# Kernel tuning notes

Measured on AMD Instinct MI355X. Metric: run time of the kernel, lower is better.

## Reference

```python
import jax, jax.numpy as jnp
import numpy as np

N_NODES = 50000
N_EDGES = 800000
D_IN = 256
D_HID = 256
N_LAYERS = 3
N_GRAPHS = 64
LN_EPS = 1e-5


def setup_inputs() -> dict:
    key = jax.random.key(0)
    ks = jax.random.split(key, 8)
    x = jax.random.normal(ks[0], (N_NODES, D_IN), dtype=jnp.float32)
    edge_index = jax.random.randint(ks[1], (2, N_EDGES), 0, N_NODES, dtype=jnp.int32)
    batch = jnp.sort(jax.random.randint(ks[2], (N_NODES,), 0, N_GRAPHS, dtype=jnp.int32))
    # GCNConv weights (glorot-ish) and biases; all layers are [D, D] since in_dim == hidden_dim
    scale = 1.0 / np.sqrt(D_IN)
    Ws = jax.random.normal(ks[3], (N_LAYERS, D_IN, D_HID), dtype=jnp.float32) * scale
    bs = jnp.zeros((N_LAYERS, D_HID), dtype=jnp.float32)
    gammas = jnp.ones((N_LAYERS, D_HID), dtype=jnp.float32)
    betas = jnp.zeros((N_LAYERS, D_HID), dtype=jnp.float32)
    return {"x": x, "edge_index": edge_index, "batch": batch,
            "Ws": Ws, "bs": bs, "gammas": gammas, "betas": betas}


def _gcn_conv(x, W, b, src, dst):
    # PyG GCNConv: h = xW; add self-loops; symmetric deg^{-1/2} normalization; scatter-add; + bias
    h = x @ W  # [N, D]
    deg = jnp.zeros((N_NODES,), dtype=x.dtype).at[dst].add(1.0) + 1.0  # +1 for self-loop
    dinv = jax.lax.rsqrt(deg)  # deg >= 1, safe
    coef = (dinv[src] * dinv[dst])[:, None]  # [E, 1]
    agg = jax.ops.segment_sum(h[src] * coef, dst, num_segments=N_NODES)
    agg = agg + h * (dinv * dinv)[:, None]  # self-loop contribution
    return agg + b


def _layer_norm(x, gamma, beta):
    mu = jnp.mean(x, axis=-1, keepdims=True)
    var = jnp.mean(jnp.square(x - mu), axis=-1, keepdims=True)
    return (x - mu) * jax.lax.rsqrt(var + LN_EPS) * gamma + beta


def reference(x, edge_index, batch, Ws, bs, gammas, betas):
    src, dst = edge_index[0], edge_index[1]
    h = x
    for l in range(N_LAYERS):
        h = _gcn_conv(h, Ws[l], bs[l], src, dst)
        h = _layer_norm(h, gammas[l], betas[l])
        h = jax.nn.relu(h)  # dropout is identity in eval mode
    # global mean pool over graphs
    sums = jax.ops.segment_sum(h, batch, num_segments=N_GRAPHS)  # [B, D]
    counts = jax.ops.segment_sum(jnp.ones((N_NODES,), dtype=h.dtype), batch, num_segments=N_GRAPHS)
    return sums / jnp.maximum(counts, 1.0)[:, None]
```

## Files before the change

kernel.cpp:

```cpp
#include <hip/hip_runtime.h>
#include <hip/hip_bf16.h>

#define N_NODES   50000
#define N_EDGES   800000
#define D         256
#define N_LAYERS  3
#define N_GRAPHS  64
#define LN_EPS    1e-5f
#define NB_SCAN   ((N_NODES + 255) / 256)

typedef __attribute__((ext_vector_type(8))) short bf16x8;
typedef __attribute__((ext_vector_type(4))) float f32x4;

__device__ __forceinline__ unsigned short f2bf(float f) {
    unsigned int u = __float_as_uint(f);
    unsigned int r = (u + 0x7FFFu + ((u >> 16) & 1u)) >> 16;
    return (unsigned short)r;
}
__device__ __forceinline__ float bf2f(unsigned short h) {
    return __uint_as_float(((unsigned int)h) << 16);
}

__global__ void k_xtobf(const float* __restrict__ x, unsigned short* __restrict__ xb) {
    int gid = blockIdx.x * blockDim.x + threadIdx.x;
    int base = gid * 8;
    if (base >= N_NODES * D) return;
    const float4* x4 = (const float4*)(x + base);
    float4 a = x4[0], b = x4[1];
    ushort4 lo, hi;
    lo.x = f2bf(a.x); lo.y = f2bf(a.y); lo.z = f2bf(a.z); lo.w = f2bf(a.w);
    hi.x = f2bf(b.x); hi.y = f2bf(b.y); hi.z = f2bf(b.z); hi.w = f2bf(b.w);
    ((ushort4*)(xb + base))[0] = lo;
    ((ushort4*)(xb + base))[1] = hi;
}

__global__ void k_wtrans(const float* __restrict__ W, unsigned short* __restrict__ Wbt) {
    int gid = blockIdx.x * blockDim.x + threadIdx.x;
    if (gid >= N_LAYERS * D * D) return;
    int l = gid >> 16;
    int rem = gid & 65535;
    int n = rem >> 8;
    int k = rem & 255;
    Wbt[(size_t)l * D * D + n * D + k] = f2bf(W[(size_t)l * D * D + k * D + n]);
}

__global__ void k_indeg(const int* __restrict__ dst, int* __restrict__ indeg) {
    int e = blockIdx.x * blockDim.x + threadIdx.x;
    if (e < N_EDGES) atomicAdd(&indeg[dst[e]], 1);
}

__global__ void k_dinv(const int* __restrict__ indeg, float* __restrict__ dinv) {
    int n = blockIdx.x * blockDim.x + threadIdx.x;
    if (n < N_NODES) dinv[n] = rsqrtf((float)(indeg[n] + 1));
}

__global__ __launch_bounds__(256) void k_bsum(const int* __restrict__ indeg, int* __restrict__ bsum) {
    int b = blockIdx.x, t = threadIdx.x;
    int i = b * 256 + t;
    int v = (i < N_NODES) ? indeg[i] : 0;
#pragma unroll
    for (int m = 32; m >= 1; m >>= 1) v += __shfl_xor(v, m);
    __shared__ int s[4];
    if ((t & 63) == 0) s[t >> 6] = v;
    __syncthreads();
    if (t == 0) bsum[b] = s[0] + s[1] + s[2] + s[3];
}

__global__ __launch_bounds__(256) void k_bscan(const int* __restrict__ bsum, int* __restrict__ bbase) {
    __shared__ int s[256];
    int t = threadIdx.x;
    int v = (t < NB_SCAN) ? bsum[t] : 0;
    s[t] = v;
    __syncthreads();
    for (int off = 1; off < 256; off <<= 1) {
        int tv = (t >= off) ? s[t - off] : 0;
        __syncthreads();
        s[t] += tv;
        __syncthreads();
    }
    if (t < NB_SCAN) bbase[t] = s[t] - v;
}

__global__ __launch_bounds__(256) void k_offsets(const int* __restrict__ indeg, const int* __restrict__ bbase,
                                                 int* __restrict__ offsets, int* __restrict__ cursor) {
    __shared__ int s[256];
    int b = blockIdx.x, t = threadIdx.x;
    int i = b * 256 + t;
    int v = (i < N_NODES) ? indeg[i] : 0;
    s[t] = v;
    __syncthreads();
    for (int off = 1; off < 256; off <<= 1) {
        int tv = (t >= off) ? s[t - off] : 0;
        __syncthreads();
        s[t] += tv;
        __syncthreads();
    }
    if (i < N_NODES) {
        int o = bbase[b] + s[t] - v;
        offsets[i] = o;
        cursor[i]  = o;
    }
}

__global__ void k_csr_fill(const int* __restrict__ src, const int* __restrict__ dst,
                           const float* __restrict__ dinv, int* __restrict__ cursor,
                           int2* __restrict__ epairs) {
    int e = blockIdx.x * blockDim.x + threadIdx.x;
    if (e >= N_EDGES) return;
    int s = src[e], d = dst[e];
    int pos = atomicAdd(&cursor[d], 1);
    float coef = dinv[s] * dinv[d];
    epairs[pos] = make_int2(s, __float_as_int(coef));
}

__global__ void k_counts_bs(const int* __restrict__ batch, int* __restrict__ counts) {
    int g = threadIdx.x;
    if (g >= N_GRAPHS) return;
    int lo = 0, hi = N_NODES;
    while (lo < hi) { int mid = (lo + hi) >> 1; if (batch[mid] < g) lo = mid + 1; else hi = mid; }
    int start = lo;
    lo = 0; hi = N_NODES;
    int g1 = g + 1;
    while (lo < hi) { int mid = (lo + hi) >> 1; if (batch[mid] < g1) lo = mid + 1; else hi = mid; }
    counts[g] = lo - start;
}

__global__ __launch_bounds__(256) void k_agg(const unsigned short* __restrict__ h,
                                             const int* __restrict__ offsets,
                                             const int* __restrict__ indeg,
                                             const float* __restrict__ dinv,
                                             const int2* __restrict__ epairs,
                                             unsigned short* __restrict__ outA) {
    int node = blockIdx.x * 4 + (threadIdx.x >> 6);
    int lane = threadIdx.x & 63;
    if (node >= N_NODES) return;
    int hw = lane >> 5;
    int dl = lane & 31;

    float di = dinv[node];
    float selfc = (hw == 0) ? di * di : 0.f;

    float acc[8];
    {
        bf16x8 v = *(const bf16x8*)(h + (size_t)node * 256 + dl * 8);
#pragma unroll
        for (int j = 0; j < 8; ++j) acc[j] = bf2f((unsigned short)v[j]) * selfc;
    }

    int beg = offsets[node];
    int end = beg + indeg[node];
    int i = beg + hw;
    for (; i + 2 < end; i += 4) {
        int2 e0 = epairs[i];
        int2 e1 = epairs[i + 2];
        bf16x8 v0 = *(const bf16x8*)(h + (size_t)e0.x * 256 + dl * 8);
        bf16x8 v1 = *(const bf16x8*)(h + (size_t)e1.x * 256 + dl * 8);
        float c0 = __int_as_float(e0.y);
        float c1 = __int_as_float(e1.y);
#pragma unroll
        for (int j = 0; j < 8; ++j) acc[j] = fmaf(bf2f((unsigned short)v0[j]), c0, acc[j]);
#pragma unroll
        for (int j = 0; j < 8; ++j) acc[j] = fmaf(bf2f((unsigned short)v1[j]), c1, acc[j]);
    }
    if (i < end) {
        int2 e0 = epairs[i];
        bf16x8 v0 = *(const bf16x8*)(h + (size_t)e0.x * 256 + dl * 8);
        float c0 = __int_as_float(e0.y);
#pragma unroll
        for (int j = 0; j < 8; ++j) acc[j] = fmaf(bf2f((unsigned short)v0[j]), c0, acc[j]);
    }

#pragma unroll
    for (int j = 0; j < 8; ++j) acc[j] += __shfl_xor(acc[j], 32);

    if (hw == 0) {
        bf16x8 o;
#pragma unroll
        for (int j = 0; j < 8; ++j) o[j] = (short)f2bf(acc[j]);
        *(bf16x8*)(outA + (size_t)node * 256 + dl * 8) = o;
    }
}

__global__ __launch_bounds__(256) void k_gemm_ln(const unsigned short* __restrict__ A,
                                                 const unsigned short* __restrict__ Wbt,
                                                 const float* __restrict__ bias,
                                                 const float* __restrict__ gamma,
                                                 const float* __restrict__ beta,
                                                 unsigned short* __restrict__ out) {
    const int t = threadIdx.x;
    const int lane = t & 63;
    const int w = t >> 6;
    const int lrow = lane & 15;
    const int q = lane >> 4;
    const int mbase = blockIdx.x * 128 + w * 32;

    f32x4 acc[2][16];
#pragma unroll
    for (int mt = 0; mt < 2; ++mt)
#pragma unroll
        for (int nt = 0; nt < 16; ++nt) acc[mt][nt] = (f32x4){0.f, 0.f, 0.f, 0.f};

    int rowA[2];
#pragma unroll
    for (int mt = 0; mt < 2; ++mt) {
        int r = mbase + mt * 16 + lrow;
        rowA[mt] = (r < N_NODES) ? r : (N_NODES - 1);
    }
    const unsigned short* a0 = A + (size_t)rowA[0] * 256 + q * 8;
    const unsigned short* a1 = A + (size_t)rowA[1] * 256 + q * 8;
    const unsigned short* wp = Wbt + (size_t)lrow * 256 + q * 8;

#pragma unroll
    for (int ks = 0; ks < 8; ++ks) {
        bf16x8 av0 = *(const bf16x8*)(a0 + ks * 32);
        bf16x8 av1 = *(const bf16x8*)(a1 + ks * 32);
#pragma unroll
        for (int nt = 0; nt < 16; ++nt) {
            bf16x8 b = *(const bf16x8*)(wp + (size_t)nt * 16 * 256 + ks * 32);
            acc[0][nt] = __builtin_amdgcn_mfma_f32_16x16x32_bf16(b, av0, acc[0][nt], 0, 0, 0);
            acc[1][nt] = __builtin_amdgcn_mfma_f32_16x16x32_bf16(b, av1, acc[1][nt], 0, 0, 0);
        }
    }

    const float4* bias4 = (const float4*)bias;
    const float4* g4 = (const float4*)gamma;
    const float4* be4 = (const float4*)beta;

#pragma unroll
    for (int mt = 0; mt < 2; ++mt) {
        float s = 0.f, s2 = 0.f;
#pragma unroll
        for (int nt = 0; nt < 16; ++nt) {
            float4 bv = bias4[nt * 4 + q];
#pragma unroll
            for (int r = 0; r < 4; ++r) {
                float v = acc[mt][nt][r] + ((const float*)&bv)[r];
                acc[mt][nt][r] = v;
                s += v;
                s2 += v * v;
            }
        }
        s  += __shfl_xor(s, 16);  s  += __shfl_xor(s, 32);
        s2 += __shfl_xor(s2, 16); s2 += __shfl_xor(s2, 32);
        float mu = s * (1.0f / 256.0f);
        float var = s2 * (1.0f / 256.0f) - mu * mu;
        float rs = rsqrtf(var + LN_EPS);

        int row = mbase + mt * 16 + lrow;
        if (row < N_NODES) {
#pragma unroll
            for (int nt = 0; nt < 16; ++nt) {
                float4 gv = g4[nt * 4 + q];
                float4 bev = be4[nt * 4 + q];
                ushort4 o;
                float v0 = fmaxf((acc[mt][nt][0] - mu) * rs * gv.x + bev.x, 0.f);
                float v1 = fmaxf((acc[mt][nt][1] - mu) * rs * gv.y + bev.y, 0.f);
                float v2 = fmaxf((acc[mt][nt][2] - mu) * rs * gv.z + bev.z, 0.f);
                float v3 = fmaxf((acc[mt][nt][3] - mu) * rs * gv.w + bev.w, 0.f);
                o.x = f2bf(v0); o.y = f2bf(v1); o.z = f2bf(v2); o.w = f2bf(v3);
                *(ushort4*)(out + (size_t)row * 256 + nt * 16 + q * 4) = o;
            }
        }
    }
}

__global__ __launch_bounds__(256) void k_pool(const unsigned short* __restrict__ h,
                                              const int* __restrict__ batch,
                                              float* __restrict__ sums) {
    __shared__ int sb[128];
    int t = threadIdx.x;
    int n0 = blockIdx.x * 128;
    int cnt = N_NODES - n0; if (cnt > 128) cnt = 128;
    if (cnt <= 0) return;
    if (t < cnt) sb[t] = batch[n0 + t];
    __syncthreads();

    float acc = 0.f;
    int g = sb[0];
    for (int i = 0; i < cnt; ++i) {
        int bg = sb[i];
        if (bg != g) {
            atomicAdd(&sums[g * 256 + t], acc);
            acc = 0.f;
            g = bg;
        }
        acc += bf2f(h[(size_t)(n0 + i) * 256 + t]);
    }
    atomicAdd(&sums[g * 256 + t], acc);
}

__global__ void k_finalize(const float* __restrict__ sums, const int* __restrict__ counts,
                           float* __restrict__ out) {
    int idx = blockIdx.x * blockDim.x + threadIdx.x;
    if (idx < N_GRAPHS * 256) {
        float c = (float)counts[idx >> 8];
        out[idx] = sums[idx] / fmaxf(c, 1.f);
    }
}

extern "C" void kernel_launch(void* const* d_in, const int* in_sizes, int n_in,
                              void* d_out, int out_size, void* d_ws, size_t ws_size,
                              hipStream_t stream) {
    const float* x     = (const float*)d_in[0];
    const int*   ei    = (const int*)d_in[1];
    const int*   batch = (const int*)d_in[2];
    const float* Ws    = (const float*)d_in[3];
    const float* bs    = (const float*)d_in[4];
    const float* gammas= (const float*)d_in[5];
    const float* betas = (const float*)d_in[6];
    float* out = (float*)d_out;

    const int* src = ei;
    const int* dst = ei + N_EDGES;

    char* p = (char*)d_ws;
    unsigned short* hbf   = (unsigned short*)p; p += (size_t)N_NODES * D * 2;
    unsigned short* aggx  = (unsigned short*)p; p += (size_t)N_NODES * D * 2;
    unsigned short* Wbt   = (unsigned short*)p; p += (size_t)N_LAYERS * D * D * 2;
    int*   indeg  = (int*)p;   p += (size_t)N_NODES * 4;
    int*   offs   = (int*)p;   p += (size_t)N_NODES * 4;
    int*   cursor = (int*)p;   p += (size_t)N_NODES * 4;
    float* dinv   = (float*)p; p += (size_t)N_NODES * 4;
    int*   bsum   = (int*)p;   p += (size_t)NB_SCAN * 4;
    int*   bbase  = (int*)p;   p += (size_t)NB_SCAN * 4;
    int2*  epairs = (int2*)p;  p += (size_t)N_EDGES * 8;
    float* sums   = (float*)p; p += (size_t)N_GRAPHS * D * 4;
    int*   counts = (int*)p;   p += (size_t)N_GRAPHS * 4;

    hipMemsetAsync(indeg, 0, (size_t)N_NODES * 4, stream);
    hipMemsetAsync(sums, 0, (size_t)N_GRAPHS * D * 4, stream);

    k_xtobf <<<(N_NODES * D / 8 + 255) / 256, 256, 0, stream>>>(x, hbf);
    k_wtrans<<<(N_LAYERS * D * D + 255) / 256, 256, 0, stream>>>(Ws, Wbt);

    k_indeg <<<(N_EDGES + 255) / 256, 256, 0, stream>>>(dst, indeg);
    k_dinv  <<<NB_SCAN, 256, 0, stream>>>(indeg, dinv);
    k_bsum  <<<NB_SCAN, 256, 0, stream>>>(indeg, bsum);
    k_bscan <<<1, 256, 0, stream>>>(bsum, bbase);
    k_offsets<<<NB_SCAN, 256, 0, stream>>>(indeg, bbase, offs, cursor);
    k_csr_fill<<<(N_EDGES + 255) / 256, 256, 0, stream>>>(src, dst, dinv, cursor, epairs);
    k_counts_bs<<<1, 64, 0, stream>>>(batch, counts);

    const int agg_grid  = (N_NODES + 3) / 4;
    const int gemm_grid = (N_NODES + 127) / 128;
    for (int l = 0; l < N_LAYERS; ++l) {
        k_agg<<<agg_grid, 256, 0, stream>>>(hbf, offs, indeg, dinv, epairs, aggx);
        k_gemm_ln<<<gemm_grid, 256, 0, stream>>>(aggx, Wbt + (size_t)l * D * D,
                                                 bs + (size_t)l * D,
                                                 gammas + (size_t)l * D,
                                                 betas + (size_t)l * D, hbf);
    }

    k_pool<<<(N_NODES + 127) / 128, 256, 0, stream>>>(hbf, batch, sums);
    k_finalize<<<(N_GRAPHS * 256 + 255) / 256, 256, 0, stream>>>(sums, counts, out);
}
```

Before: 486.4 us.

## Factor GCN normalization into row scaling and split aggregation by feature slices

The symmetric normalization is factored out of the edges. Node features are pre-scaled by dinv, either in the input conversion or in the LayerNorm epilogue of the previous layer, and the aggregated sum is scaled by dinv of the destination node. This removes the per-edge coefficient, so the CSR holds only 16-bit source indices instead of int2 (index, coef) pairs, which cuts edge-list traffic. The aggregation kernel is reorganised so each block handles one 32-column slice of 4 nodes and spreads 16 edges per wave, with a cross-lane shuffle reduction at the end. The trade-offs are narrower 64-byte gathers per edge, extra shuffle work, and an index format that only works while the node count stays below 65536.

```diff
diff --git a/kernel.cpp b/kernel.cpp
--- a/kernel.cpp
+++ b/kernel.cpp
@@ -21,15 +21,17 @@
     return __uint_as_float(((unsigned int)h) << 16);
 }
 
-__global__ void k_xtobf(const float* __restrict__ x, unsigned short* __restrict__ xb) {
+__global__ void k_xtobf_s(const float* __restrict__ x, const float* __restrict__ dinv,
+                          unsigned short* __restrict__ xb) {
     int gid = blockIdx.x * blockDim.x + threadIdx.x;
     int base = gid * 8;
     if (base >= N_NODES * D) return;
+    float sc = dinv[base >> 8];
     const float4* x4 = (const float4*)(x + base);
     float4 a = x4[0], b = x4[1];
     ushort4 lo, hi;
-    lo.x = f2bf(a.x); lo.y = f2bf(a.y); lo.z = f2bf(a.z); lo.w = f2bf(a.w);
-    hi.x = f2bf(b.x); hi.y = f2bf(b.y); hi.z = f2bf(b.z); hi.w = f2bf(b.w);
+    lo.x = f2bf(a.x * sc); lo.y = f2bf(a.y * sc); lo.z = f2bf(a.z * sc); lo.w = f2bf(a.w * sc);
+    hi.x = f2bf(b.x * sc); hi.y = f2bf(b.y * sc); hi.z = f2bf(b.z * sc); hi.w = f2bf(b.w * sc);
     ((ushort4*)(xb + base))[0] = lo;
     ((ushort4*)(xb + base))[1] = hi;
 }
@@ -103,14 +105,12 @@
 }
 
 __global__ void k_csr_fill(const int* __restrict__ src, const int* __restrict__ dst,
-                           const float* __restrict__ dinv, int* __restrict__ cursor,
-                           int2* __restrict__ epairs) {
+                           int* __restrict__ cursor, unsigned short* __restrict__ esrc) {
     int e = blockIdx.x * blockDim.x + threadIdx.x;
     if (e >= N_EDGES) return;
     int s = src[e], d = dst[e];
     int pos = atomicAdd(&cursor[d], 1);
-    float coef = dinv[s] * dinv[d];
-    epairs[pos] = make_int2(s, __float_as_int(coef));
+    esrc[pos] = (unsigned short)s;
 }
 
 __global__ void k_counts_bs(const int* __restrict__ batch, int* __restrict__ counts) {
@@ -129,55 +129,46 @@
                                              const int* __restrict__ offsets,
                                              const int* __restrict__ indeg,
                                              const float* __restrict__ dinv,
-                                             const int2* __restrict__ epairs,
+                                             const unsigned short* __restrict__ esrc,
                                              unsigned short* __restrict__ outA) {
-    int node = blockIdx.x * 4 + (threadIdx.x >> 6);
-    int lane = threadIdx.x & 63;
+    const int part = blockIdx.x & 7;
+    const int node = (blockIdx.x >> 3) * 4 + (threadIdx.x >> 6);
     if (node >= N_NODES) return;
-    int hw = lane >> 5;
-    int dl = lane & 31;
-
-    float di = dinv[node];
-    float selfc = (hw == 0) ? di * di : 0.f;
+    const int lane = threadIdx.x & 63;
+    const int eg = lane >> 2;
+    const int dl = lane & 3;
+    const unsigned short* hp = h + part * 32 + dl * 8;
 
     float acc[8];
-    {
-        bf16x8 v = *(const bf16x8*)(h + (size_t)node * 256 + dl * 8);
-#pragma unroll
-        for (int j = 0; j < 8; ++j) acc[j] = bf2f((unsigned short)v[j]) * selfc;
-    }
-
-    int beg = offsets[node];
-    int end = beg + indeg[node];
-    int i = beg + hw;
-    for (; i + 2 < end; i += 4) {
-        int2 e0 = epairs[i];
-        int2 e1 = epairs[i + 2];
-        bf16x8 v0 = *(const bf16x8*)(h + (size_t)e0.x * 256 + dl * 8);
-        bf16x8 v1 = *(const bf16x8*)(h + (size_t)e1.x * 256 + dl * 8);
-        float c0 = __int_as_float(e0.y);
-        float c1 = __int_as_float(e1.y);
-#pragma unroll
-        for (int j = 0; j < 8; ++j) acc[j] = fmaf(bf2f((unsigned short)v0[j]), c0, acc[j]);
-#pragma unroll
-        for (int j = 0; j < 8; ++j) acc[j] = fmaf(bf2f((unsigned short)v1[j]), c1, acc[j]);
-    }
-    if (i < end) {
-        int2 e0 = epairs[i];
-        bf16x8 v0 = *(const bf16x8*)(h + (size_t)e0.x * 256 + dl * 8);
-        float c0 = __int_as_float(e0.y);
-#pragma unroll
-        for (int j = 0; j < 8; ++j) acc[j] = fmaf(bf2f((unsigned short)v0[j]), c0, acc[j]);
-    }
-
-#pragma unroll
-    for (int j = 0; j < 8; ++j) acc[j] += __shfl_xor(acc[j], 32);
-
-    if (hw == 0) {
+    if (eg == 0) {
+        bf16x8 v = *(const bf16x8*)(hp + (size_t)node * 256);
+#pragma unroll
+        for (int j = 0; j < 8; ++j) acc[j] = bf2f((unsigned short)v[j]);
+    } else {
+#pragma unroll
+        for (int j = 0; j < 8; ++j) acc[j] = 0.f;
+    }
+
+    const int beg = offsets[node];
+    const int end = beg + indeg[node];
+    for (int i = beg + eg; i < end; i += 16) {
+        int s = esrc[i];
+        bf16x8 v = *(const bf16x8*)(hp + (size_t)s * 256);
+#pragma unroll
+        for (int j = 0; j < 8; ++j) acc[j] += bf2f((unsigned short)v[j]);
+    }
+
+#pragma unroll
+    for (int m = 4; m <= 32; m <<= 1)
+#pragma unroll
+        for (int j = 0; j < 8; ++j) acc[j] += __shfl_xor(acc[j], m);
+
+    if (eg == 0) {
+        float sc = dinv[node];
         bf16x8 o;
 #pragma unroll
-        for (int j = 0; j < 8; ++j) o[j] = (short)f2bf(acc[j]);
-        *(bf16x8*)(outA + (size_t)node * 256 + dl * 8) = o;
+        for (int j = 0; j < 8; ++j) o[j] = (short)f2bf(acc[j] * sc);
+        *(bf16x8*)(outA + (size_t)node * 256 + part * 32 + dl * 8) = o;
     }
 }
 
@@ -186,6 +177,7 @@
                                                  const float* __restrict__ bias,
                                                  const float* __restrict__ gamma,
                                                  const float* __restrict__ beta,
+                                                 const float* __restrict__ rowscale,
                                                  unsigned short* __restrict__ out) {
     const int t = threadIdx.x;
     const int lane = t & 63;
@@ -248,15 +240,16 @@
 
         int row = mbase + mt * 16 + lrow;
         if (row < N_NODES) {
+            float sc = (rowscale != nullptr) ? rowscale[row] : 1.0f;
 #pragma unroll
             for (int nt = 0; nt < 16; ++nt) {
                 float4 gv = g4[nt * 4 + q];
                 float4 bev = be4[nt * 4 + q];
                 ushort4 o;
-                float v0 = fmaxf((acc[mt][nt][0] - mu) * rs * gv.x + bev.x, 0.f);
-                float v1 = fmaxf((acc[mt][nt][1] - mu) * rs * gv.y + bev.y, 0.f);
-                float v2 = fmaxf((acc[mt][nt][2] - mu) * rs * gv.z + bev.z, 0.f);
-                float v3 = fmaxf((acc[mt][nt][3] - mu) * rs * gv.w + bev.w, 0.f);
+                float v0 = fmaxf((acc[mt][nt][0] - mu) * rs * gv.x + bev.x, 0.f) * sc;
+                float v1 = fmaxf((acc[mt][nt][1] - mu) * rs * gv.y + bev.y, 0.f) * sc;
+                float v2 = fmaxf((acc[mt][nt][2] - mu) * rs * gv.z + bev.z, 0.f) * sc;
+                float v3 = fmaxf((acc[mt][nt][3] - mu) * rs * gv.w + bev.w, 0.f) * sc;
                 o.x = f2bf(v0); o.y = f2bf(v1); o.z = f2bf(v2); o.w = f2bf(v3);
                 *(ushort4*)(out + (size_t)row * 256 + nt * 16 + q * 4) = o;
             }
@@ -323,32 +316,32 @@
     float* dinv   = (float*)p; p += (size_t)N_NODES * 4;
     int*   bsum   = (int*)p;   p += (size_t)NB_SCAN * 4;
     int*   bbase  = (int*)p;   p += (size_t)NB_SCAN * 4;
-    int2*  epairs = (int2*)p;  p += (size_t)N_EDGES * 8;
+    unsigned short* esrc = (unsigned short*)p; p += (size_t)N_EDGES * 2;
     float* sums   = (float*)p; p += (size_t)N_GRAPHS * D * 4;
     int*   counts = (int*)p;   p += (size_t)N_GRAPHS * 4;
 
     hipMemsetAsync(indeg, 0, (size_t)N_NODES * 4, stream);
     hipMemsetAsync(sums, 0, (size_t)N_GRAPHS * D * 4, stream);
 
-    k_xtobf <<<(N_NODES * D / 8 + 255) / 256, 256, 0, stream>>>(x, hbf);
-    k_wtrans<<<(N_LAYERS * D * D + 255) / 256, 256, 0, stream>>>(Ws, Wbt);
-
     k_indeg <<<(N_EDGES + 255) / 256, 256, 0, stream>>>(dst, indeg);
     k_dinv  <<<NB_SCAN, 256, 0, stream>>>(indeg, dinv);
+    k_xtobf_s<<<(N_NODES * D / 8 + 255) / 256, 256, 0, stream>>>(x, dinv, hbf);
+    k_wtrans<<<(N_LAYERS * D * D + 255) / 256, 256, 0, stream>>>(Ws, Wbt);
     k_bsum  <<<NB_SCAN, 256, 0, stream>>>(indeg, bsum);
     k_bscan <<<1, 256, 0, stream>>>(bsum, bbase);
     k_offsets<<<NB_SCAN, 256, 0, stream>>>(indeg, bbase, offs, cursor);
-    k_csr_fill<<<(N_EDGES + 255) / 256, 256, 0, stream>>>(src, dst, dinv, cursor, epairs);
+    k_csr_fill<<<(N_EDGES + 255) / 256, 256, 0, stream>>>(src, dst, cursor, esrc);
     k_counts_bs<<<1, 64, 0, stream>>>(batch, counts);
 
-    const int agg_grid  = (N_NODES + 3) / 4;
+    const int agg_grid  = ((N_NODES + 3) / 4) * 8;
     const int gemm_grid = (N_NODES + 127) / 128;
     for (int l = 0; l < N_LAYERS; ++l) {
-        k_agg<<<agg_grid, 256, 0, stream>>>(hbf, offs, indeg, dinv, epairs, aggx);
+        k_agg<<<agg_grid, 256, 0, stream>>>(hbf, offs, indeg, dinv, esrc, aggx);
+        const float* rsc = (l == N_LAYERS - 1) ? nullptr : dinv;
         k_gemm_ln<<<gemm_grid, 256, 0, stream>>>(aggx, Wbt + (size_t)l * D * D,
                                                  bs + (size_t)l * D,
                                                  gammas + (size_t)l * D,
-                                                 betas + (size_t)l * D, hbf);
+                                                 betas + (size_t)l * D, rsc, hbf);
     }
 
     k_pool<<<(N_NODES + 127) / 128, 256, 0, stream>>>(hbf, batch, sums);
```

New measurement: 841.4 us. +73.0%, slower.
